# Kernel tuning notes

Hardware: AMD Instinct MI355X
Metric: run time of the kernel (lower is better)

The kernel has to match this reference:

```python
import jax, jax.numpy as jnp
import numpy as np

N, M, E = 100000, 500, 300000
XS, GS, OUT, HEADS = 100, 100, 100, 2
SLOPE = 0.2
EPS = 1e-12


def l2norm(x, axis):
    n = jnp.linalg.norm(x, axis=axis, keepdims=True)
    return x / jnp.maximum(n, EPS)


def gat_layer(h_ijk, ends, n, W, att):
    # W: [heads*out, in_dim] (no bias); att: [1, heads, out]
    heads, out = att.shape[1], att.shape[2]
    c = (h_ijk @ W.T).reshape(-1, heads, out)               # [E, H, D]
    a = jnp.sum(att * c, axis=2, keepdims=True)             # [E, H, 1]
    e = jnp.exp(-jax.nn.leaky_relu(a, SLOPE))
    denom = jax.ops.segment_sum(e, ends, num_segments=n)    # [n, H, 1]
    alpha = e / denom[ends]                                 # segment softmax (dropout=eval/identity)
    h = jax.ops.segment_sum(alpha * c, ends, num_segments=n)  # [n, H, D]
    h = jax.nn.elu(h)
    h = l2norm(h, axis=2)
    return h.reshape(n, heads * out)


def merge_layer(h_in, h_out, Wi, bi, Wo, bo, Wl, bl):
    hi = h_in @ Wi.T + bi
    ho = h_out @ Wo.T + bo
    lam = jax.nn.sigmoid(jnp.concatenate([hi, ho], axis=1) @ Wl.T + bl)
    h = lam * hi + (1.0 - lam) * ho
    return l2norm(jax.nn.elu(h), axis=1)


def setup_inputs() -> dict:
    key = jax.random.key(0)
    ks = jax.random.split(key, 24)
    D = HEADS * OUT  # 200
    in1 = 2 * XS + GS   # 300
    in2 = 3 * D         # 600
    s = 0.05
    return {
        'edge_idx': jax.random.randint(ks[0], (2, E), 0, N),
        'edge_type': jax.random.randint(ks[1], (E,), 0, M),
        'path_idx': jax.random.randint(ks[2], (2, 8), 0, N),
        'path_type': jax.random.randint(ks[3], (2, 8), 0, M),
        'use_path': 0,
        'x': jax.random.normal(ks[4], (N, XS), jnp.float32),
        'g': jax.random.normal(ks[5], (M, GS), jnp.float32),
        'W_in1': s * jax.random.normal(ks[6], (D, in1), jnp.float32),
        'att_in1': s * jax.random.normal(ks[7], (1, HEADS, OUT), jnp.float32),
        'W_out1': s * jax.random.normal(ks[8], (D, in1), jnp.float32),
        'att_out1': s * jax.random.normal(ks[9], (1, HEADS, OUT), jnp.float32),
        'Wi1': s * jax.random.normal(ks[10], (D, D), jnp.float32), 'bi1': jnp.zeros((D,), jnp.float32),
        'Wo1': s * jax.random.normal(ks[11], (D, D), jnp.float32), 'bo1': jnp.zeros((D,), jnp.float32),
        'Wl1': s * jax.random.normal(ks[12], (1, 2 * D), jnp.float32), 'bl1': jnp.zeros((1,), jnp.float32),
        'Wr': s * jax.random.normal(ks[13], (D, GS), jnp.float32), 'br': jnp.zeros((D,), jnp.float32),
        'Wf': s * jax.random.normal(ks[14], (D, in1), jnp.float32), 'bf': jnp.zeros((D,), jnp.float32),
        'W_in2': s * jax.random.normal(ks[15], (D, in2), jnp.float32),
        'att_in2': s * jax.random.normal(ks[16], (1, 1, D), jnp.float32),
        'W_out2': s * jax.random.normal(ks[17], (D, in2), jnp.float32),
        'att_out2': s * jax.random.normal(ks[18], (1, 1, D), jnp.float32),
        'Wi2': s * jax.random.normal(ks[19], (D, D), jnp.float32), 'bi2': jnp.zeros((D,), jnp.float32),
        'Wo2': s * jax.random.normal(ks[20], (D, D), jnp.float32), 'bo2': jnp.zeros((D,), jnp.float32),
        'Wl2': s * jax.random.normal(ks[21], (1, 2 * D), jnp.float32), 'bl2': jnp.zeros((1,), jnp.float32),
        'W_ent': s * jax.random.normal(ks[22], (D, XS), jnp.float32),
    }


def reference(edge_idx, edge_type, path_idx, path_type, use_path, x, g,
              W_in1, att_in1, W_out1, att_out1, Wi1, bi1, Wo1, bo1, Wl1, bl1,
              Wr, br, Wf, bf,
              W_in2, att_in2, W_out2, att_out2, Wi2, bi2, Wo2, bo2, Wl2, bl2,
              W_ent):
    n, m = x.shape[0], g.shape[0]
    x = l2norm(x, axis=1)  # x_initial is renormalized each forward
    row, col = edge_idx[0], edge_idx[1]
    # hop 1: gather-concat per-edge features [E, 2*XS+GS]
    h_ijk = jnp.concatenate([x[row], x[col], g[edge_type]], axis=1)
    h_in = gat_layer(h_ijk, col, n, W_in1, att_in1)
    h_out = gat_layer(h_ijk, row, n, W_out1, att_out1)
    h = merge_layer(h_in, h_out, Wi1, bi1, Wo1, bo1, Wl1, bl1)
    # relation layer
    g_edges = jax.ops.segment_sum(h_ijk, edge_type, num_segments=m)
    g_edges = jax.nn.elu(l2norm(g_edges, axis=1))
    g_prime = (g @ Wr.T + br) + (g_edges @ Wf.T + bf)
    # hop 2
    h_ijk2 = jnp.concatenate([h[row], h[col], g_prime[edge_type]], axis=1)
    h_in2 = gat_layer(h_ijk2, col, n, W_in2, att_in2)
    h_out2 = gat_layer(h_ijk2, row, n, W_out2, att_out2)
    h = merge_layer(h_in2, h_out2, Wi2, bi2, Wo2, bo2, Wl2, bl2)
    # entity residual layer
    h_prime = x @ W_ent.T + h
    return h_prime
```

## Files before the change

### kernel.cpp

```cpp
#include <hip/hip_runtime.h>
#include <cstddef>
#include <cstdint>

#define WSLOPE 0.2f
#define WEPS 1e-12f

typedef __attribute__((ext_vector_type(8))) short bf16x8;
typedef __attribute__((ext_vector_type(4))) float f32x4;

__device__ __forceinline__ float waveSum(float v) {
#pragma unroll
    for (int off = 32; off > 0; off >>= 1) v += __shfl_xor(v, off, 64);
    return v;
}
__device__ __forceinline__ float rowSum16(float v) {
#pragma unroll
    for (int off = 8; off > 0; off >>= 1) v += __shfl_xor(v, off, 64);
    return v;
}
__device__ __forceinline__ float eluf(float v) { return v > 0.f ? v : expm1f(v); }
__device__ __forceinline__ short f2bf(float f) {
    union { float f; uint32_t u; } v; v.f = f;
    uint32_t r = v.u + 0x7FFF + ((v.u >> 16) & 1);
    return (short)(r >> 16);
}
__device__ __forceinline__ float bf2f(short s) {
    union { uint32_t u; float f; } v; v.u = ((uint32_t)(uint16_t)s) << 16;
    return v.f;
}

__global__ void k_nodeprep(const float* __restrict__ x, float* __restrict__ invn,
                           short* __restrict__ xnb,
                           const float* __restrict__ wai, const float* __restrict__ wao,
                           float* __restrict__ rdi, float* __restrict__ cdi,
                           float* __restrict__ rdo, float* __restrict__ cdo, int N) {
    int wid = blockIdx.x * 4 + (threadIdx.x >> 6);
    int lane = threadIdx.x & 63;
    if (wid >= N) return;
    const float* p = x + (size_t)wid * 100;
    float a0 = p[lane];
    float a1 = (lane < 36) ? p[lane + 64] : 0.f;
    float ss = waveSum(a0 * a0 + a1 * a1);
    float inv = 1.f / fmaxf(sqrtf(ss), WEPS);
    if (lane == 0) invn[wid] = inv;
    float f0 = a0 * inv, f1 = a1 * inv;
    short* xb = xnb + (size_t)wid * 112;
    xb[lane] = f2bf(f0);
    if (lane < 36) xb[64 + lane] = f2bf(f1);
    else if (lane < 48) xb[64 + lane] = 0;
#pragma unroll
    for (int h = 0; h < 2; ++h) {
        const float* wi = wai + h * 300;
        const float* wo = wao + h * 300;
        float ri = f0 * wi[lane] + f1 * wi[lane + 64];
        float ci = f0 * wi[100 + lane] + f1 * wi[100 + lane + 64];
        float ro = f0 * wo[lane] + f1 * wo[lane + 64];
        float co = f0 * wo[100 + lane] + f1 * wo[100 + lane + 64];
        ri = waveSum(ri); ci = waveSum(ci); ro = waveSum(ro); co = waveSum(co);
        if (lane == 0) { rdi[wid * 2 + h] = ri; cdi[wid * 2 + h] = ci; rdo[wid * 2 + h] = ro; cdo[wid * 2 + h] = co; }
    }
}

__global__ void k_gprep(const float* __restrict__ g, short* __restrict__ gbf,
                        short* __restrict__ gcomb,
                        const float* __restrict__ wai, const float* __restrict__ wao,
                        float* __restrict__ gdi, float* __restrict__ gdo, int M) {
    int m = blockIdx.x * 4 + (threadIdx.x >> 6);
    int lane = threadIdx.x & 63;
    if (m >= M) return;
    const float* gm = g + (size_t)m * 100;
    float v0 = gm[lane];
    float v1 = (lane < 36) ? gm[lane + 64] : 0.f;
    short b0 = f2bf(v0), b1 = (lane < 36) ? f2bf(v1) : (short)0;
    short* gb = gbf + (size_t)m * 112;
    gb[lane] = b0;
    if (lane < 48) gb[64 + lane] = (lane < 36) ? b1 : (short)0;
    short* gc = gcomb + (size_t)m * 448;
    gc[lane] = b0;
    gc[64 + lane] = b1;
    float s0 = v0 * wai[200 + lane];
    float s1 = v0 * wai[500 + lane];
    float s2 = v0 * wao[200 + lane];
    float s3 = v0 * wao[500 + lane];
    if (lane < 36) {
        s0 += v1 * wai[264 + lane]; s1 += v1 * wai[564 + lane];
        s2 += v1 * wao[264 + lane]; s3 += v1 * wao[564 + lane];
    }
    s0 = waveSum(s0); s1 = waveSum(s1); s2 = waveSum(s2); s3 = waveSum(s3);
    if (lane == 0) { gdi[m * 2] = s0; gdi[m * 2 + 1] = s1; gdo[m * 2] = s2; gdo[m * 2 + 1] = s3; }
}

__global__ void k_count(const int* __restrict__ keys, int* __restrict__ cnt, int n) {
    int i = blockIdx.x * 256 + threadIdx.x;
    if (i < n) atomicAdd(&cnt[keys[i]], 1);
}

#define SCAN_CHUNK 2048
__global__ void k_blocksum(const int* __restrict__ cnt, int* __restrict__ bsum, int n) {
    __shared__ int sh[256];
    int b = blockIdx.x, t = threadIdx.x;
    int base = b * SCAN_CHUNK;
    int s = 0;
    for (int i = t; i < SCAN_CHUNK; i += 256) { int idx = base + i; if (idx < n) s += cnt[idx]; }
    sh[t] = s; __syncthreads();
    for (int off = 128; off > 0; off >>= 1) { if (t < off) sh[t] += sh[t + off]; __syncthreads(); }
    if (t == 0) bsum[b] = sh[0];
}

__global__ void k_scanwrite(const int* __restrict__ cnt, const int* __restrict__ bsum,
                            int* __restrict__ offs, int* __restrict__ cur, int n, int nb) {
    __shared__ int sh[256];
    __shared__ int sbase;
    int b = blockIdx.x, t = threadIdx.x;
    if (t == 0) { int s = 0; for (int i = 0; i < b; ++i) s += bsum[i]; sbase = s; }
    __syncthreads();
    int base = b * SCAN_CHUNK;
    int loc[8]; int ts = 0;
#pragma unroll
    for (int i = 0; i < 8; ++i) { int idx = base + t * 8 + i; int v = (idx < n) ? cnt[idx] : 0; loc[i] = ts; ts += v; }
    sh[t] = ts; __syncthreads();
    for (int off = 1; off < 256; off <<= 1) {
        int v = (t >= off) ? sh[t - off] : 0;
        __syncthreads();
        sh[t] += v;
        __syncthreads();
    }
    int excl = (t == 0) ? 0 : sh[t - 1];
    int gbase = sbase + excl;
#pragma unroll
    for (int i = 0; i < 8; ++i) {
        int idx = base + t * 8 + i;
        if (idx < n) { offs[idx] = gbase + loc[i]; cur[idx] = gbase + loc[i]; }
    }
    if (b == nb - 1 && t == 255) offs[n] = sbase + sh[255];
}

__global__ void k_scatter3(const int* __restrict__ keys, const int* __restrict__ other,
                           const int* __restrict__ et, int* __restrict__ cur,
                           int* __restrict__ nbrS, int* __restrict__ etS,
                           int* __restrict__ keyS, int n) {
    int i = blockIdx.x * 256 + threadIdx.x;
    if (i < n) {
        int p = atomicAdd(&cur[keys[i]], 1);
        nbrS[p] = other[i];
        etS[p] = et[i];
        keyS[p] = keys[i];
    }
}

__global__ void k_scatter2(const int* __restrict__ keys, int* __restrict__ cur,
                           int* __restrict__ rs, int* __restrict__ cs,
                           const int* __restrict__ row, const int* __restrict__ col, int n) {
    int i = blockIdx.x * 256 + threadIdx.x;
    if (i < n) {
        int p = atomicAdd(&cur[keys[i]], 1);
        rs[p] = row[i];
        cs[p] = col[i];
    }
}

__global__ void k_watt(const float* __restrict__ att, const float* __restrict__ W,
                       float* __restrict__ wa, int H, int DH, int K) {
    int id = blockIdx.x * 256 + threadIdx.x;
    if (id >= H * K) return;
    int h = id / K, k = id % K;
    float s = 0.f;
    for (int j = 0; j < DH; ++j) s += att[h * DH + j] * W[(size_t)(h * DH + j) * K + k];
    wa[id] = s;
}

__global__ void k_ew2(const int* __restrict__ nbi, const int* __restrict__ kyi,
                      const int* __restrict__ eti,
                      const int* __restrict__ nbo, const int* __restrict__ kyo,
                      const int* __restrict__ eto,
                      const float* __restrict__ rdi, const float* __restrict__ cdi,
                      const float* __restrict__ rdo, const float* __restrict__ cdo,
                      const float* __restrict__ gdi, const float* __restrict__ gdo,
                      float* __restrict__ ewi, float* __restrict__ ewo, int E, int H) {
    int id = blockIdx.x * 256 + threadIdx.x;
    int tot = E * H;
    if (id >= 2 * tot) return;
    if (id < tot) {
        int p = id / H, h = id - p * H;
        float a = rdi[nbi[p] * H + h] + cdi[kyi[p] * H + h] + gdi[eti[p] * H + h];
        float lr = a > 0.f ? a : WSLOPE * a;
        ewi[id] = expf(-lr);
    } else {
        int id2 = id - tot;
        int p = id2 / H, h = id2 - p * H;
        float a = cdo[nbo[p] * H + h] + rdo[kyo[p] * H + h] + gdo[eto[p] * H + h];
        float lr = a > 0.f ? a : WSLOPE * a;
        ewo[id2] = expf(-lr);
    }
}

template<bool HOP2>
__global__ void k_agg(const int* __restrict__ offs, const int* __restrict__ nbrS,
                      const int* __restrict__ etS, const float* __restrict__ ewS,
                      const short* __restrict__ featB, const short* __restrict__ gB,
                      short* __restrict__ A, int n0, int n1) {
    constexpr int H = HOP2 ? 1 : 2;
    constexpr int LDA = HOP2 ? 672 : 576;
    constexpr int FW = HOP2 ? 224 : 112;
    constexpr int GW = HOP2 ? 224 : 112;
    int node = n0 + blockIdx.x * 4 + (threadIdx.x >> 6);
    int lane = threadIdx.x & 63;
    if (node >= n1) return;
    int o = offs[node];
    int deg = offs[node + 1] - o;
    float va[7];
#pragma unroll
    for (int m = 0; m < 7; ++m) va[m] = 0.f;
    if (deg > 0) {
        float s0 = 0.f, s1 = 0.f;
        for (int i = lane; i < deg; i += 64) {
            s0 += ewS[(size_t)(o + i) * H];
            if (H == 2) s1 += ewS[(size_t)(o + i) * H + 1];
        }
        s0 = waveSum(s0);
        float rd0 = 1.f / s0, rd1 = rd0;
        if (H == 2) { s1 = waveSum(s1); rd1 = 1.f / s1; }
        for (int j = 0; j < deg; ++j) {
            float a0 = ewS[(size_t)(o + j) * H] * rd0;
            float a1 = (H == 2) ? ewS[(size_t)(o + j) * H + 1] * rd1 : a0;
            int nbr = nbrS[o + j];
            int et = etS[o + j];
            const short* fr = featB + (size_t)nbr * FW;
            const short* gr = gB + (size_t)et * GW;
            if (!HOP2) {
#pragma unroll
                for (int m = 0; m < 7; ++m) {
                    int d = lane + m * 64;
                    if (d < 100) va[m] += a0 * bf2f(fr[d]);
                    else if (d < 200) va[m] += a1 * bf2f(fr[d - 100]);
                    else if (d < 300) va[m] += a0 * bf2f(gr[d - 200]);
                    else if (d < 400) va[m] += a1 * bf2f(gr[d - 300]);
                }
            } else {
#pragma unroll
                for (int m = 0; m < 7; ++m) {
                    int d = lane + m * 64;
                    if (d < 200) va[m] += a0 * bf2f(fr[d]);
                    else if (d < 424) va[m] += a0 * bf2f(gr[d - 200]);
                }
            }
        }
    }
    size_t rb = (size_t)(node - n0);
    short* Ar = A + rb * LDA;
    if (!HOP2) {
#pragma unroll
        for (int m = 0; m < 7; ++m) {
            int d = lane + m * 64;
            if (d < 400) {
                int col = d < 100 ? d : (d < 200 ? d + 12 : (d < 300 ? d + 24 : d + 36));
                Ar[col] = f2bf(va[m]);
            }
        }
        if (lane < 48) { int q = lane / 12; int rm = lane - q * 12; Ar[q * 112 + 100 + rm] = 0; }
        const short* sf = featB + (size_t)node * 112;
#pragma unroll
        for (int mm = 0; mm < 2; ++mm) {
            int k = lane + mm * 64;
            if (k < 128) Ar[448 + k] = (deg > 0 && k < 112) ? sf[k] : (short)0;
        }
    } else {
#pragma unroll
        for (int m = 0; m < 7; ++m) {
            int d = lane + m * 64;
            if (d < 424) Ar[d < 200 ? d : d + 24] = f2bf(va[m]);
        }
        if (lane < 24) Ar[200 + lane] = 0;
        const short* sf = featB + (size_t)node * 224;
#pragma unroll
        for (int mm = 0; mm < 4; ++mm) {
            int k = lane + mm * 64;
            if (k < 224) Ar[448 + k] = deg > 0 ? sf[k] : (short)0;
        }
    }
}

template<int KSTEPS, int H, bool HOP1>
__launch_bounds__(256)
__global__ void k_gatmerge(const short* __restrict__ Ain, const short* __restrict__ Aout,
                           const short* __restrict__ WcA, const short* __restrict__ WcB,
                           const short* __restrict__ Wi, const short* __restrict__ Wo,
                           const float* __restrict__ bi, const float* __restrict__ bo,
                           const float* __restrict__ Wl, const float* __restrict__ bl,
                           const short* __restrict__ xnb, const short* __restrict__ Went,
                           float* __restrict__ outf, short* __restrict__ h1b,
                           const float* __restrict__ wa2i, const float* __restrict__ wa2o,
                           float* __restrict__ rdi, float* __restrict__ cdi,
                           float* __restrict__ rdo, float* __restrict__ cdo,
                           int rows) {
    constexpr int LDA = KSTEPS * 32;
    __shared__ short pL[2][64][232];
    const int t = threadIdx.x;
    const int wv = t >> 6, l = t & 63;
    const int lhi = l >> 4, llo = l & 15;
    const int rbase = blockIdx.x * 64 + wv * 16;

#pragma unroll 1
    for (int dir = 0; dir < 2; ++dir) {
        const short* A = dir ? Aout : Ain;
        const short* Wc = dir ? WcB : WcA;
        f32x4 acc[13];
#pragma unroll
        for (int j = 0; j < 13; ++j) acc[j] = f32x4{0.f, 0.f, 0.f, 0.f};
        const short* arow = A + (size_t)(rbase + llo) * LDA + lhi * 8;
#pragma unroll
        for (int kt = 0; kt < KSTEPS; ++kt) {
            bf16x8 a = *(const bf16x8*)(arow + kt * 32);
#pragma unroll
            for (int j = 0; j < 13; ++j) {
                bf16x8 b = *(const bf16x8*)(Wc + (size_t)(j * 16 + llo) * LDA + kt * 32 + lhi * 8);
                acc[j] = __builtin_amdgcn_mfma_f32_16x16x32_bf16(a, b, acc[j], 0, 0, 0);
            }
        }
#pragma unroll
        for (int e = 0; e < 4; ++e) {
            float v[13];
            float s0 = 0.f, s1 = 0.f;
#pragma unroll
            for (int j = 0; j < 13; ++j) {
                int d = j * 16 + llo;
                if (d < 200) {
                    float xv = eluf(acc[j][e]);
                    v[j] = xv;
                    if (H == 1 || d < 100) s0 += xv * xv; else s1 += xv * xv;
                }
            }
            s0 = rowSum16(s0);
            float inv0 = 1.f / fmaxf(sqrtf(s0), WEPS);
            float inv1 = inv0;
            if (H == 2) { s1 = rowSum16(s1); inv1 = 1.f / fmaxf(sqrtf(s1), WEPS); }
            short* pr = &pL[dir][wv * 16 + lhi * 4 + e][0];
#pragma unroll
            for (int j = 0; j < 13; ++j) {
                int d = j * 16 + llo;
                if (d < 200) pr[d] = f2bf(v[j] * ((H == 2 && d >= 100) ? inv1 : inv0));
                else pr[d] = 0;
            }
            pr[208 + llo] = 0;
        }
    }
    __syncthreads();

    f32x4 accA[13], accB[13];
#pragma unroll
    for (int j = 0; j < 13; ++j) { accA[j] = f32x4{0.f, 0.f, 0.f, 0.f}; accB[j] = f32x4{0.f, 0.f, 0.f, 0.f}; }
    const short* pa = &pL[0][wv * 16 + llo][0];
    const short* pb = &pL[1][wv * 16 + llo][0];
#pragma unroll
    for (int kt = 0; kt < 7; ++kt) {
        bf16x8 a1 = *(const bf16x8*)(pa + kt * 32 + lhi * 8);
        bf16x8 a2 = *(const bf16x8*)(pb + kt * 32 + lhi * 8);
#pragma unroll
        for (int j = 0; j < 13; ++j) {
            bf16x8 b1 = *(const bf16x8*)(Wi + (size_t)(j * 16 + llo) * 224 + kt * 32 + lhi * 8);
            accA[j] = __builtin_amdgcn_mfma_f32_16x16x32_bf16(a1, b1, accA[j], 0, 0, 0);
            bf16x8 b2 = *(const bf16x8*)(Wo + (size_t)(j * 16 + llo) * 224 + kt * 32 + lhi * 8);
            accB[j] = __builtin_amdgcn_mfma_f32_16x16x32_bf16(a2, b2, accB[j], 0, 0, 0);
        }
    }
    f32x4 accR[13];
    if (!HOP1) {
#pragma unroll
        for (int j = 0; j < 13; ++j) accR[j] = f32x4{0.f, 0.f, 0.f, 0.f};
        const short* xr = xnb + (size_t)(rbase + llo) * 112 + lhi * 8;
#pragma unroll
        for (int kt = 0; kt < 4; ++kt) {
            bf16x8 a = *(const bf16x8*)(xr + kt * 32);
#pragma unroll
            for (int j = 0; j < 13; ++j) {
                bf16x8 b = *(const bf16x8*)(Went + (size_t)(j * 16 + llo) * 128 + kt * 32 + lhi * 8);
                accR[j] = __builtin_amdgcn_mfma_f32_16x16x32_bf16(a, b, accR[j], 0, 0, 0);
            }
        }
    }

    const int r0 = rbase + lhi * 4;
    float blv = bl[0];
#pragma unroll
    for (int e = 0; e < 4; ++e) {
        int r = r0 + e;
        if (r >= rows) continue;
        float vi[13], vo[13];
        float lp = 0.f;
#pragma unroll
        for (int j = 0; j < 13; ++j) {
            int d = j * 16 + llo;
            if (d < 200) {
                vi[j] = accA[j][e] + bi[d];
                vo[j] = accB[j][e] + bo[d];
                lp += Wl[d] * vi[j] + Wl[200 + d] * vo[j];
            }
        }
        lp = rowSum16(lp);
        float lam = 1.f / (1.f + expf(-(lp + blv)));
        float hv[13];
        float ss = 0.f;
#pragma unroll
        for (int j = 0; j < 13; ++j) {
            int d = j * 16 + llo;
            if (d < 200) { hv[j] = eluf(lam * vi[j] + (1.f - lam) * vo[j]); ss += hv[j] * hv[j]; }
        }
        ss = rowSum16(ss);
        float inv = 1.f / fmaxf(sqrtf(ss), WEPS);
        float ri = 0.f, ci = 0.f, ro = 0.f, co = 0.f;
#pragma unroll
        for (int j = 0; j < 13; ++j) {
            int d = j * 16 + llo;
            if (d < 200) {
                float val = hv[j] * inv;
                if (HOP1) {
                    h1b[(size_t)r * 224 + d] = f2bf(val);
                    ri += val * wa2i[d]; ci += val * wa2i[200 + d];
                    ro += val * wa2o[d]; co += val * wa2o[200 + d];
                } else {
                    outf[(size_t)r * 200 + d] = val + accR[j][e];
                }
            } else if (HOP1) {
                h1b[(size_t)r * 224 + d] = 0;
            }
        }
        if (HOP1) {
            h1b[(size_t)r * 224 + 208 + llo] = 0;
            ri = rowSum16(ri); ci = rowSum16(ci); ro = rowSum16(ro); co = rowSum16(co);
            if (llo == 0) { rdi[r] = ri; cdi[r] = ci; rdo[r] = ro; cdo[r] = co; }
        }
    }
}

__launch_bounds__(256)
__global__ void k_mgemm_rel(const short* __restrict__ A, const short* __restrict__ Wb,
                            const float* __restrict__ brf,
                            short* __restrict__ gout, const float* __restrict__ wai,
                            const float* __restrict__ wao,
                            float* __restrict__ gdi, float* __restrict__ gdo, int rows) {
    constexpr int KSTEPS = 14, LDW = KSTEPS * 32;
    const int t = threadIdx.x;
    const int wv = t >> 6, l = t & 63;
    const int lhi = l >> 4, llo = l & 15;
    const int rbase = blockIdx.x * 64 + wv * 16;
    f32x4 acc[13];
#pragma unroll
    for (int j = 0; j < 13; ++j) acc[j] = f32x4{0.f, 0.f, 0.f, 0.f};
    const short* arow = A + (size_t)(rbase + llo) * 448 + lhi * 8;
#pragma unroll
    for (int kt = 0; kt < KSTEPS; ++kt) {
        bf16x8 a = *(const bf16x8*)(arow + kt * 32);
#pragma unroll
        for (int j = 0; j < 13; ++j) {
            bf16x8 b = *(const bf16x8*)(Wb + (size_t)(j * 16 + llo) * LDW + kt * 32 + lhi * 8);
            acc[j] = __builtin_amdgcn_mfma_f32_16x16x32_bf16(a, b, acc[j], 0, 0, 0);
        }
    }
    const int r0 = rbase + lhi * 4;
#pragma unroll
    for (int e = 0; e < 4; ++e) {
        int r = r0 + e;
        if (r >= rows) continue;
        short* pr = gout + (size_t)r * 224;
        float gi = 0.f, go = 0.f;
#pragma unroll
        for (int j = 0; j < 13; ++j) {
            int d = j * 16 + llo;
            if (d < 200) {
                float val = acc[j][e] + brf[d];
                pr[d] = f2bf(val);
                gi += val * wai[400 + d];
                go += val * wao[400 + d];
            } else {
                pr[d] = 0;
            }
        }
        pr[208 + llo] = 0;
        gi = rowSum16(gi); go = rowSum16(go);
        if (llo == 0) { gdi[r] = gi; gdo[r] = go; }
    }
}

__global__ void k_prepw(const float* __restrict__ W, int ldW, int koff, int Klen, int span,
                        int mode, short* __restrict__ Wb, int ldWb, int dst) {
    int id = blockIdx.x * 256 + threadIdx.x;
    int tot = 208 * span;
    if (id >= tot) return;
    int d = id / span, k = id - d * span;
    float v = 0.f;
    if (d < 200) {
        if (mode == 0) { if (k < Klen) v = W[(size_t)d * ldW + koff + k]; }
        else { int h = d / 100; int kk = k - h * 112; if (kk >= 0 && kk < Klen) v = W[(size_t)d * ldW + koff + kk]; }
    }
    Wb[(size_t)d * ldWb + dst + k] = f2bf(v);
}

__global__ void k_prepwrf(const float* __restrict__ Wr, const float* __restrict__ Wf,
                          short* __restrict__ Wb) {
    int id = blockIdx.x * 256 + threadIdx.x;
    if (id >= 208 * 448) return;
    int d = id / 448, k = id - d * 448;
    float v = 0.f;
    if (d < 200) {
        if (k < 100) v = Wr[(size_t)d * 100 + k];
        else if (k >= 128 && k < 428) v = Wf[(size_t)d * 300 + (k - 128)];
    }
    Wb[id] = f2bf(v);
}

__global__ void k_brf(const float* __restrict__ br, const float* __restrict__ bf,
                      float* __restrict__ brf) {
    int d = threadIdx.x;
    if (d < 200) brf[d] = br[d] + bf[d];
}

__global__ void k_gedges_b(const int* __restrict__ rsT, const int* __restrict__ csT,
                           const int* __restrict__ offsT,
                           const float* __restrict__ x, const float* __restrict__ invn,
                           const float* __restrict__ g, short* __restrict__ gcomb, int M) {
    __shared__ float red[6];
    int m = blockIdx.x, t = threadIdx.x;
    int o = offsT[m];
    int deg = offsT[m + 1] - o;
    float acc = 0.f;
    if (t < 128) {
        int d = t; bool ok = d < 100;
        for (int i = 0; i < deg; ++i) {
            int r = rsT[o + i];
            if (ok) acc += x[(size_t)r * 100 + d] * invn[r];
        }
    } else if (t < 256) {
        int d = t - 128; bool ok = d < 100;
        for (int i = 0; i < deg; ++i) {
            int c = csT[o + i];
            if (ok) acc += x[(size_t)c * 100 + d] * invn[c];
        }
    } else {
        int d = t - 256;
        if (d < 100) acc = (float)deg * g[(size_t)m * 100 + d];
    }
    float sq = waveSum(acc * acc);
    if ((t & 63) == 0) red[t >> 6] = sq;
    __syncthreads();
    float s2 = red[0] + red[1] + red[2] + red[3] + red[4] + red[5];
    float inv = 1.f / fmaxf(sqrtf(s2), WEPS);
    short* orow = gcomb + (size_t)m * 448 + 128;
    if (t < 128) {
        if (t < 100) orow[t] = f2bf(eluf(acc * inv));
    } else if (t < 256) {
        int d = t - 128;
        if (d < 100) orow[100 + d] = f2bf(eluf(acc * inv));
    } else {
        int d = t - 256;
        if (d < 100) orow[200 + d] = f2bf(eluf(acc * inv));
        else if (d < 120) orow[200 + d] = 0;
    }
}

extern "C" void kernel_launch(void* const* d_in, const int* in_sizes, int n_in,
                              void* d_out, int out_size, void* d_ws, size_t ws_size,
                              hipStream_t stream) {
    const int* eidx   = (const int*)d_in[0];
    const int* etype  = (const int*)d_in[1];
    const float* x    = (const float*)d_in[5];
    const float* g    = (const float*)d_in[6];
    const float* W_in1  = (const float*)d_in[7];
    const float* att_in1 = (const float*)d_in[8];
    const float* W_out1 = (const float*)d_in[9];
    const float* att_out1 = (const float*)d_in[10];
    const float* Wi1 = (const float*)d_in[11]; const float* bi1 = (const float*)d_in[12];
    const float* Wo1 = (const float*)d_in[13]; const float* bo1 = (const float*)d_in[14];
    const float* Wl1 = (const float*)d_in[15]; const float* bl1 = (const float*)d_in[16];
    const float* Wr  = (const float*)d_in[17]; const float* br  = (const float*)d_in[18];
    const float* Wf  = (const float*)d_in[19]; const float* bf  = (const float*)d_in[20];
    const float* W_in2  = (const float*)d_in[21]; const float* att_in2 = (const float*)d_in[22];
    const float* W_out2 = (const float*)d_in[23]; const float* att_out2 = (const float*)d_in[24];
    const float* Wi2 = (const float*)d_in[25]; const float* bi2 = (const float*)d_in[26];
    const float* Wo2 = (const float*)d_in[27]; const float* bo2 = (const float*)d_in[28];
    const float* Wl2 = (const float*)d_in[29]; const float* bl2 = (const float*)d_in[30];
    const float* W_ent = (const float*)d_in[31];

    const int E = in_sizes[1];
    const int N = in_sizes[5] / 100;
    const int M = in_sizes[6] / 100;
    const int Mr = (M + 63) & ~63;
    float* out = (float*)d_out;
    const int* row = eidx;
    const int* col = eidx + E;

    char* w = (char*)d_ws;
    size_t off_b = 0;
    auto alloc = [&](size_t bytes) -> void* {
        void* p = w + off_b;
        off_b += (bytes + 255) & ~(size_t)255;
        return p;
    };
    float* invn  = (float*)alloc((size_t)N * 4);
    short* h1_bf = (short*)alloc((size_t)(N + 64) * 224 * 2);
    short* xn_bf = (short*)alloc((size_t)(N + 64) * 112 * 2);
    short* g_bf  = (short*)alloc((size_t)M * 112 * 2);
    short* gp_bf = (short*)alloc((size_t)Mr * 224 * 2);
    int* offs_in = (int*)alloc((size_t)(N + 1) * 4);
    int* offs_out= (int*)alloc((size_t)(N + 1) * 4);
    int* offsT   = (int*)alloc((size_t)(M + 1) * 4);
    int* nbrS_in = (int*)alloc((size_t)E * 4);
    int* etS_in  = (int*)alloc((size_t)E * 4);
    int* keyS_in = (int*)alloc((size_t)E * 4);
    int* nbrS_out= (int*)alloc((size_t)E * 4);
    int* etS_out = (int*)alloc((size_t)E * 4);
    int* keyS_out= (int*)alloc((size_t)E * 4);
    int* rsT     = (int*)alloc((size_t)E * 4);
    int* csT     = (int*)alloc((size_t)E * 4);
    int* cnt     = (int*)alloc((size_t)N * 4);
    int* cur     = (int*)alloc((size_t)N * 4);
    int* bsum    = (int*)alloc((size_t)64 * 4);
    float* wa1_in = (float*)alloc((size_t)640 * 4);
    float* wa1_out= (float*)alloc((size_t)640 * 4);
    float* wa2_in = (float*)alloc((size_t)640 * 4);
    float* wa2_out= (float*)alloc((size_t)640 * 4);
    float* rdot_in = (float*)alloc((size_t)N * 2 * 4);
    float* cdot_in = (float*)alloc((size_t)N * 2 * 4);
    float* rdot_out= (float*)alloc((size_t)N * 2 * 4);
    float* cdot_out= (float*)alloc((size_t)N * 2 * 4);
    float* gdot_in = (float*)alloc((size_t)M * 2 * 4);
    float* gdot_out= (float*)alloc((size_t)M * 2 * 4);
    float* ewS_in  = (float*)alloc((size_t)E * 2 * 4);
    float* ewS_out = (float*)alloc((size_t)E * 2 * 4);
    short* gcomb   = (short*)alloc((size_t)Mr * 448 * 2);
    short* Wc_in1  = (short*)alloc((size_t)208 * 576 * 2);
    short* Wc_out1 = (short*)alloc((size_t)208 * 576 * 2);
    short* Wc_in2  = (short*)alloc((size_t)208 * 672 * 2);
    short* Wc_out2 = (short*)alloc((size_t)208 * 672 * 2);
    short* Wm_i1   = (short*)alloc((size_t)208 * 224 * 2);
    short* Wm_o1   = (short*)alloc((size_t)208 * 224 * 2);
    short* Wm_i2   = (short*)alloc((size_t)208 * 224 * 2);
    short* Wm_o2   = (short*)alloc((size_t)208 * 224 * 2);
    short* Wb_ent  = (short*)alloc((size_t)208 * 128 * 2);
    short* Wrf_b   = (short*)alloc((size_t)208 * 448 * 2);
    float* brf     = (float*)alloc((size_t)200 * 4);

    if (off_b >= ws_size) return;
    size_t rem = ws_size - off_b;
    long long Cll = (long long)(rem / 2816);
    long long Nr64 = ((long long)N + 63) & ~63LL;
    int C = (int)(Cll > Nr64 ? Nr64 : Cll);
    C &= ~63;
    if (C < 64) return;
    short* Ac0 = (short*)alloc((size_t)C * 672 * 2);
    short* Ac1 = (short*)alloc((size_t)C * 672 * 2);
    if (off_b > ws_size) return;

    const int gE = (E + 255) / 256;
    const int gN4 = (N + 3) / 4;
    const int gM4 = (M + 3) / 4;
    const int gM64 = (M + 63) / 64;

    auto gsp = [](int span) { return (208 * span + 255) / 256; };
    k_prepw<<<gsp(224), 256, 0, stream>>>(W_in1, 300, 0, 100, 224, 1, Wc_in1, 576, 0);
    k_prepw<<<gsp(224), 256, 0, stream>>>(W_in1, 300, 200, 100, 224, 1, Wc_in1, 576, 224);
    k_prepw<<<gsp(128), 256, 0, stream>>>(W_in1, 300, 100, 100, 128, 0, Wc_in1, 576, 448);
    k_prepw<<<gsp(224), 256, 0, stream>>>(W_out1, 300, 100, 100, 224, 1, Wc_out1, 576, 0);
    k_prepw<<<gsp(224), 256, 0, stream>>>(W_out1, 300, 200, 100, 224, 1, Wc_out1, 576, 224);
    k_prepw<<<gsp(128), 256, 0, stream>>>(W_out1, 300, 0, 100, 128, 0, Wc_out1, 576, 448);
    k_prepw<<<gsp(224), 256, 0, stream>>>(W_in2, 600, 0, 200, 224, 0, Wc_in2, 672, 0);
    k_prepw<<<gsp(224), 256, 0, stream>>>(W_in2, 600, 400, 200, 224, 0, Wc_in2, 672, 224);
    k_prepw<<<gsp(224), 256, 0, stream>>>(W_in2, 600, 200, 200, 224, 0, Wc_in2, 672, 448);
    k_prepw<<<gsp(224), 256, 0, stream>>>(W_out2, 600, 200, 200, 224, 0, Wc_out2, 672, 0);
    k_prepw<<<gsp(224), 256, 0, stream>>>(W_out2, 600, 400, 200, 224, 0, Wc_out2, 672, 224);
    k_prepw<<<gsp(224), 256, 0, stream>>>(W_out2, 600, 0, 200, 224, 0, Wc_out2, 672, 448);
    k_prepw<<<gsp(224), 256, 0, stream>>>(Wi1, 200, 0, 200, 224, 0, Wm_i1, 224, 0);
    k_prepw<<<gsp(224), 256, 0, stream>>>(Wo1, 200, 0, 200, 224, 0, Wm_o1, 224, 0);
    k_prepw<<<gsp(224), 256, 0, stream>>>(Wi2, 200, 0, 200, 224, 0, Wm_i2, 224, 0);
    k_prepw<<<gsp(224), 256, 0, stream>>>(Wo2, 200, 0, 200, 224, 0, Wm_o2, 224, 0);
    k_prepw<<<gsp(128), 256, 0, stream>>>(W_ent, 100, 0, 100, 128, 0, Wb_ent, 128, 0);
    k_prepwrf<<<gsp(448), 256, 0, stream>>>(Wr, Wf, Wrf_b);
    k_brf<<<1, 256, 0, stream>>>(br, bf, brf);

    int nbN = (N + SCAN_CHUNK - 1) / SCAN_CHUNK;
    int nbM = (M + SCAN_CHUNK - 1) / SCAN_CHUNK;
    hipMemsetAsync(cnt, 0, (size_t)N * 4, stream);
    k_count<<<gE, 256, 0, stream>>>(col, cnt, E);
    k_blocksum<<<nbN, 256, 0, stream>>>(cnt, bsum, N);
    k_scanwrite<<<nbN, 256, 0, stream>>>(cnt, bsum, offs_in, cur, N, nbN);
    k_scatter3<<<gE, 256, 0, stream>>>(col, row, etype, cur, nbrS_in, etS_in, keyS_in, E);

    hipMemsetAsync(cnt, 0, (size_t)N * 4, stream);
    k_count<<<gE, 256, 0, stream>>>(row, cnt, E);
    k_blocksum<<<nbN, 256, 0, stream>>>(cnt, bsum, N);
    k_scanwrite<<<nbN, 256, 0, stream>>>(cnt, bsum, offs_out, cur, N, nbN);
    k_scatter3<<<gE, 256, 0, stream>>>(row, col, etype, cur, nbrS_out, etS_out, keyS_out, E);

    hipMemsetAsync(cnt, 0, (size_t)M * 4, stream);
    k_count<<<gE, 256, 0, stream>>>(etype, cnt, E);
    k_blocksum<<<nbM, 256, 0, stream>>>(cnt, bsum, M);
    k_scanwrite<<<nbM, 256, 0, stream>>>(cnt, bsum, offsT, cur, M, nbM);
    k_scatter2<<<gE, 256, 0, stream>>>(etype, cur, rsT, csT, row, col, E);

    k_watt<<<(600 + 255) / 256, 256, 0, stream>>>(att_in1, W_in1, wa1_in, 2, 100, 300);
    k_watt<<<(600 + 255) / 256, 256, 0, stream>>>(att_out1, W_out1, wa1_out, 2, 100, 300);
    k_watt<<<(600 + 255) / 256, 256, 0, stream>>>(att_in2, W_in2, wa2_in, 1, 200, 600);
    k_watt<<<(600 + 255) / 256, 256, 0, stream>>>(att_out2, W_out2, wa2_out, 1, 200, 600);

    k_nodeprep<<<gN4, 256, 0, stream>>>(x, invn, xn_bf, wa1_in, wa1_out,
                                        rdot_in, cdot_in, rdot_out, cdot_out, N);
    k_gprep<<<gM4, 256, 0, stream>>>(g, g_bf, gcomb, wa1_in, wa1_out, gdot_in, gdot_out, M);
    k_ew2<<<(2 * E * 2 + 255) / 256, 256, 0, stream>>>(nbrS_in, keyS_in, etS_in,
                                                       nbrS_out, keyS_out, etS_out,
                                                       rdot_in, cdot_in, rdot_out, cdot_out,
                                                       gdot_in, gdot_out, ewS_in, ewS_out, E, 2);

    for (int n0 = 0; n0 < N; n0 += C) {
        int rows = (N - n0 < C) ? (N - n0) : C;
        int n1 = n0 + rows;
        int ga = (rows + 3) / 4;
        int gb = (rows + 63) / 64;
        k_agg<false><<<ga, 256, 0, stream>>>(offs_in, nbrS_in, etS_in, ewS_in, xn_bf, g_bf, Ac0, n0, n1);
        k_agg<false><<<ga, 256, 0, stream>>>(offs_out, nbrS_out, etS_out, ewS_out, xn_bf, g_bf, Ac1, n0, n1);
        k_gatmerge<18, 2, true><<<gb, 256, 0, stream>>>(Ac0, Ac1, Wc_in1, Wc_out1, Wm_i1, Wm_o1,
                                                        bi1, bo1, Wl1, bl1, nullptr, nullptr,
                                                        nullptr, h1_bf + (size_t)n0 * 224,
                                                        wa2_in, wa2_out,
                                                        rdot_in + n0, cdot_in + n0,
                                                        rdot_out + n0, cdot_out + n0, rows);
    }

    k_gedges_b<<<M, 384, 0, stream>>>(rsT, csT, offsT, x, invn, g, gcomb, M);
    k_mgemm_rel<<<gM64, 256, 0, stream>>>(gcomb, Wrf_b, brf, gp_bf, wa2_in, wa2_out, gdot_in, gdot_out, M);

    k_ew2<<<(2 * E + 255) / 256, 256, 0, stream>>>(nbrS_in, keyS_in, etS_in,
                                                   nbrS_out, keyS_out, etS_out,
                                                   rdot_in, cdot_in, rdot_out, cdot_out,
                                                   gdot_in, gdot_out, ewS_in, ewS_out, E, 1);

    for (int n0 = 0; n0 < N; n0 += C) {
        int rows = (N - n0 < C) ? (N - n0) : C;
        int n1 = n0 + rows;
        int ga = (rows + 3) / 4;
        int gb = (rows + 63) / 64;
        k_agg<true><<<ga, 256, 0, stream>>>(offs_in, nbrS_in, etS_in, ewS_in, h1_bf, gp_bf, Ac0, n0, n1);
        k_agg<true><<<ga, 256, 0, stream>>>(offs_out, nbrS_out, etS_out, ewS_out, h1_bf, gp_bf, Ac1, n0, n1);
        k_gatmerge<21, 1, false><<<gb, 256, 0, stream>>>(Ac0, Ac1, Wc_in2, Wc_out2, Wm_i2, Wm_o2,
                                                         bi2, bo2, Wl2, bl2,
                                                         xn_bf + (size_t)n0 * 112, Wb_ent,
                                                         out + (size_t)n0 * 200, nullptr,
                                                         nullptr, nullptr,
                                                         nullptr, nullptr, nullptr, nullptr, rows);
    }
}
```

Before: 3.079 ms.

## Split fused GAT+merge kernel into per-direction GEMM and column-split merge kernel

```diff
diff --git a/kernel.cpp b/kernel.cpp
--- a/kernel.cpp
+++ b/kernel.cpp
@@ -280,10 +280,60 @@
     }
 }
 
-template<int KSTEPS, int H, bool HOP1>
+template<int KSTEPS, int H>
 __launch_bounds__(256)
-__global__ void k_gatmerge(const short* __restrict__ Ain, const short* __restrict__ Aout,
-                           const short* __restrict__ WcA, const short* __restrict__ WcB,
+__global__ void k_mgemm_post(const short* __restrict__ A, const short* __restrict__ Wb,
+                             short* __restrict__ post, int rows, int lda) {
+    constexpr int LDW = KSTEPS * 32;
+    const int t = threadIdx.x;
+    const int wv = t >> 6, l = t & 63;
+    const int lhi = l >> 4, llo = l & 15;
+    const int rbase = blockIdx.x * 64 + wv * 16;
+    f32x4 acc[13];
+#pragma unroll
+    for (int j = 0; j < 13; ++j) acc[j] = f32x4{0.f, 0.f, 0.f, 0.f};
+    const short* arow = A + (size_t)(rbase + llo) * lda + lhi * 8;
+#pragma unroll
+    for (int kt = 0; kt < KSTEPS; ++kt) {
+        bf16x8 a = *(const bf16x8*)(arow + kt * 32);
+#pragma unroll
+        for (int j = 0; j < 13; ++j) {
+            bf16x8 b = *(const bf16x8*)(Wb + (size_t)(j * 16 + llo) * LDW + kt * 32 + lhi * 8);
+            acc[j] = __builtin_amdgcn_mfma_f32_16x16x32_bf16(a, b, acc[j], 0, 0, 0);
+        }
+    }
+    const int r0 = rbase + lhi * 4;
+#pragma unroll
+    for (int e = 0; e < 4; ++e) {
+        int r = r0 + e;
+        if (r >= rows) continue;
+        float v[13];
+        float s0 = 0.f, s1 = 0.f;
+#pragma unroll
+        for (int j = 0; j < 13; ++j) {
+            int d = j * 16 + llo;
+            if (d < 200) {
+                float xv = eluf(acc[j][e]);
+                v[j] = xv;
+                if (H == 1 || d < 100) s0 += xv * xv; else s1 += xv * xv;
+            }
+        }
+        s0 = rowSum16(s0);
+        float inv0 = 1.f / fmaxf(sqrtf(s0), WEPS);
+        float inv1 = inv0;
+        if (H == 2) { s1 = rowSum16(s1); inv1 = 1.f / fmaxf(sqrtf(s1), WEPS); }
+        short* pr = post + (size_t)r * 224;
+#pragma unroll
+        for (int j = 0; j < 13; ++j) {
+            int d = j * 16 + llo;
+            if (d < 200) pr[d] = f2bf(v[j] * ((H == 2 && d >= 100) ? inv1 : inv0));
+        }
+    }
+}
+
+template<bool HOP1>
+__launch_bounds__(512)
+__global__ void k_mergemm2(const short* __restrict__ pA, const short* __restrict__ pB,
                            const short* __restrict__ Wi, const short* __restrict__ Wo,
                            const float* __restrict__ bi, const float* __restrict__ bo,
                            const float* __restrict__ Wl, const float* __restrict__ bl,
@@ -293,126 +343,104 @@
                            float* __restrict__ rdi, float* __restrict__ cdi,
                            float* __restrict__ rdo, float* __restrict__ cdo,
                            int rows) {
-    constexpr int LDA = KSTEPS * 32;
-    __shared__ short pL[2][64][232];
+    __shared__ float lpS[2][64];
+    __shared__ float ssS[2][64];
+    __shared__ float dotS[2][64][4];
     const int t = threadIdx.x;
-    const int wv = t >> 6, l = t & 63;
+    const int wvAll = t >> 6;
+    const int rg = wvAll >> 1;
+    const int half = wvAll & 1;
+    const int l = t & 63;
     const int lhi = l >> 4, llo = l & 15;
-    const int rbase = blockIdx.x * 64 + wv * 16;
-
-#pragma unroll 1
-    for (int dir = 0; dir < 2; ++dir) {
-        const short* A = dir ? Aout : Ain;
-        const short* Wc = dir ? WcB : WcA;
-        f32x4 acc[13];
-#pragma unroll
-        for (int j = 0; j < 13; ++j) acc[j] = f32x4{0.f, 0.f, 0.f, 0.f};
-        const short* arow = A + (size_t)(rbase + llo) * LDA + lhi * 8;
-#pragma unroll
-        for (int kt = 0; kt < KSTEPS; ++kt) {
-            bf16x8 a = *(const bf16x8*)(arow + kt * 32);
-#pragma unroll
-            for (int j = 0; j < 13; ++j) {
-                bf16x8 b = *(const bf16x8*)(Wc + (size_t)(j * 16 + llo) * LDA + kt * 32 + lhi * 8);
-                acc[j] = __builtin_amdgcn_mfma_f32_16x16x32_bf16(a, b, acc[j], 0, 0, 0);
-            }
-        }
-#pragma unroll
-        for (int e = 0; e < 4; ++e) {
-            float v[13];
-            float s0 = 0.f, s1 = 0.f;
-#pragma unroll
-            for (int j = 0; j < 13; ++j) {
-                int d = j * 16 + llo;
-                if (d < 200) {
-                    float xv = eluf(acc[j][e]);
-                    v[j] = xv;
-                    if (H == 1 || d < 100) s0 += xv * xv; else s1 += xv * xv;
-                }
-            }
-            s0 = rowSum16(s0);
-            float inv0 = 1.f / fmaxf(sqrtf(s0), WEPS);
-            float inv1 = inv0;
-            if (H == 2) { s1 = rowSum16(s1); inv1 = 1.f / fmaxf(sqrtf(s1), WEPS); }
-            short* pr = &pL[dir][wv * 16 + lhi * 4 + e][0];
-#pragma unroll
-            for (int j = 0; j < 13; ++j) {
-                int d = j * 16 + llo;
-                if (d < 200) pr[d] = f2bf(v[j] * ((H == 2 && d >= 100) ? inv1 : inv0));
-                else pr[d] = 0;
-            }
-            pr[208 + llo] = 0;
-        }
-    }
-    __syncthreads();
-
-    f32x4 accA[13], accB[13];
-#pragma unroll
-    for (int j = 0; j < 13; ++j) { accA[j] = f32x4{0.f, 0.f, 0.f, 0.f}; accB[j] = f32x4{0.f, 0.f, 0.f, 0.f}; }
-    const short* pa = &pL[0][wv * 16 + llo][0];
-    const short* pb = &pL[1][wv * 16 + llo][0];
+    const int jbase = half * 7;
+    const int rbase = blockIdx.x * 64 + rg * 16;
+    f32x4 accA[7], accB[7];
+#pragma unroll
+    for (int j = 0; j < 7; ++j) { accA[j] = f32x4{0.f, 0.f, 0.f, 0.f}; accB[j] = f32x4{0.f, 0.f, 0.f, 0.f}; }
+    const short* pa = pA + (size_t)(rbase + llo) * 224 + lhi * 8;
+    const short* pb = pB + (size_t)(rbase + llo) * 224 + lhi * 8;
 #pragma unroll
     for (int kt = 0; kt < 7; ++kt) {
-        bf16x8 a1 = *(const bf16x8*)(pa + kt * 32 + lhi * 8);
-        bf16x8 a2 = *(const bf16x8*)(pb + kt * 32 + lhi * 8);
-#pragma unroll
-        for (int j = 0; j < 13; ++j) {
-            bf16x8 b1 = *(const bf16x8*)(Wi + (size_t)(j * 16 + llo) * 224 + kt * 32 + lhi * 8);
-            accA[j] = __builtin_amdgcn_mfma_f32_16x16x32_bf16(a1, b1, accA[j], 0, 0, 0);
-            bf16x8 b2 = *(const bf16x8*)(Wo + (size_t)(j * 16 + llo) * 224 + kt * 32 + lhi * 8);
-            accB[j] = __builtin_amdgcn_mfma_f32_16x16x32_bf16(a2, b2, accB[j], 0, 0, 0);
-        }
-    }
-    f32x4 accR[13];
+        bf16x8 a1 = *(const bf16x8*)(pa + kt * 32);
+        bf16x8 a2 = *(const bf16x8*)(pb + kt * 32);
+#pragma unroll
+        for (int j = 0; j < 7; ++j) {
+            if (jbase + j < 13) {
+                bf16x8 b1 = *(const bf16x8*)(Wi + (size_t)((jbase + j) * 16 + llo) * 224 + kt * 32 + lhi * 8);
+                accA[j] = __builtin_amdgcn_mfma_f32_16x16x32_bf16(a1, b1, accA[j], 0, 0, 0);
+                bf16x8 b2 = *(const bf16x8*)(Wo + (size_t)((jbase + j) * 16 + llo) * 224 + kt * 32 + lhi * 8);
+                accB[j] = __builtin_amdgcn_mfma_f32_16x16x32_bf16(a2, b2, accB[j], 0, 0, 0);
+            }
+        }
+    }
+    f32x4 accR[7];
     if (!HOP1) {
 #pragma unroll
-        for (int j = 0; j < 13; ++j) accR[j] = f32x4{0.f, 0.f, 0.f, 0.f};
+        for (int j = 0; j < 7; ++j) accR[j] = f32x4{0.f, 0.f, 0.f, 0.f};
         const short* xr = xnb + (size_t)(rbase + llo) * 112 + lhi * 8;
 #pragma unroll
         for (int kt = 0; kt < 4; ++kt) {
             bf16x8 a = *(const bf16x8*)(xr + kt * 32);
 #pragma unroll
-            for (int j = 0; j < 13; ++j) {
-                bf16x8 b = *(const bf16x8*)(Went + (size_t)(j * 16 + llo) * 128 + kt * 32 + lhi * 8);
-                accR[j] = __builtin_amdgcn_mfma_f32_16x16x32_bf16(a, b, accR[j], 0, 0, 0);
-            }
-        }
-    }
-
+            for (int j = 0; j < 7; ++j) {
+                if (jbase + j < 13) {
+                    bf16x8 b = *(const bf16x8*)(Went + (size_t)((jbase + j) * 16 + llo) * 128 + kt * 32 + lhi * 8);
+                    accR[j] = __builtin_amdgcn_mfma_f32_16x16x32_bf16(a, b, accR[j], 0, 0, 0);
+                }
+            }
+        }
+    }
     const int r0 = rbase + lhi * 4;
+    const int rrb = rg * 16 + lhi * 4;
     float blv = bl[0];
+#pragma unroll
+    for (int e = 0; e < 4; ++e) {
+        float lp = 0.f;
+#pragma unroll
+        for (int j = 0; j < 7; ++j) {
+            int d = (jbase + j) * 16 + llo;
+            if (jbase + j < 13 && d < 200)
+                lp += Wl[d] * (accA[j][e] + bi[d]) + Wl[200 + d] * (accB[j][e] + bo[d]);
+        }
+        lp = rowSum16(lp);
+        if (llo == 0) lpS[half][rrb + e] = lp;
+    }
+    __syncthreads();
+    float lamAll[4];
+#pragma unroll
+    for (int e = 0; e < 4; ++e) {
+        float lam = 1.f / (1.f + expf(-(lpS[0][rrb + e] + lpS[1][rrb + e] + blv)));
+        lamAll[e] = lam;
+        float ss = 0.f;
+#pragma unroll
+        for (int j = 0; j < 7; ++j) {
+            int d = (jbase + j) * 16 + llo;
+            if (jbase + j < 13 && d < 200) {
+                float vi = accA[j][e] + bi[d];
+                float vo = accB[j][e] + bo[d];
+                float hv = eluf(lam * vi + (1.f - lam) * vo);
+                ss += hv * hv;
+            }
+        }
+        ss = rowSum16(ss);
+        if (llo == 0) ssS[half][rrb + e] = ss;
+    }
+    __syncthreads();
 #pragma unroll
     for (int e = 0; e < 4; ++e) {
         int r = r0 + e;
         if (r >= rows) continue;
-        float vi[13], vo[13];
-        float lp = 0.f;
-#pragma unroll
-        for (int j = 0; j < 13; ++j) {
-            int d = j * 16 + llo;
+        float inv = 1.f / fmaxf(sqrtf(ssS[0][rrb + e] + ssS[1][rrb + e]), WEPS);
+        float lam = lamAll[e];
+        float ri = 0.f, ci = 0.f, ro = 0.f, co = 0.f;
+#pragma unroll
+        for (int j = 0; j < 7; ++j) {
+            if (jbase + j >= 13) continue;
+            int d = (jbase + j) * 16 + llo;
             if (d < 200) {
-                vi[j] = accA[j][e] + bi[d];
-                vo[j] = accB[j][e] + bo[d];
-                lp += Wl[d] * vi[j] + Wl[200 + d] * vo[j];
-            }
-        }
-        lp = rowSum16(lp);
-        float lam = 1.f / (1.f + expf(-(lp + blv)));
-        float hv[13];
-        float ss = 0.f;
-#pragma unroll
-        for (int j = 0; j < 13; ++j) {
-            int d = j * 16 + llo;
-            if (d < 200) { hv[j] = eluf(lam * vi[j] + (1.f - lam) * vo[j]); ss += hv[j] * hv[j]; }
-        }
-        ss = rowSum16(ss);
-        float inv = 1.f / fmaxf(sqrtf(ss), WEPS);
-        float ri = 0.f, ci = 0.f, ro = 0.f, co = 0.f;
-#pragma unroll
-        for (int j = 0; j < 13; ++j) {
-            int d = j * 16 + llo;
-            if (d < 200) {
-                float val = hv[j] * inv;
+                float vi = accA[j][e] + bi[d];
+                float vo = accB[j][e] + bo[d];
+                float val = eluf(lam * vi + (1.f - lam) * vo) * inv;
                 if (HOP1) {
                     h1b[(size_t)r * 224 + d] = f2bf(val);
                     ri += val * wa2i[d]; ci += val * wa2i[200 + d];
@@ -425,9 +453,27 @@
             }
         }
         if (HOP1) {
-            h1b[(size_t)r * 224 + 208 + llo] = 0;
+            if (half) h1b[(size_t)r * 224 + 208 + llo] = 0;
             ri = rowSum16(ri); ci = rowSum16(ci); ro = rowSum16(ro); co = rowSum16(co);
-            if (llo == 0) { rdi[r] = ri; cdi[r] = ci; rdo[r] = ro; cdo[r] = co; }
+            if (llo == 0) {
+                dotS[half][rrb + e][0] = ri; dotS[half][rrb + e][1] = ci;
+                dotS[half][rrb + e][2] = ro; dotS[half][rrb + e][3] = co;
+            }
+        }
+    }
+    if (HOP1) {
+        __syncthreads();
+        if (half == 0 && llo == 0) {
+#pragma unroll
+            for (int e = 0; e < 4; ++e) {
+                int r = r0 + e;
+                if (r < rows) {
+                    rdi[r] = dotS[0][rrb + e][0] + dotS[1][rrb + e][0];
+                    cdi[r] = dotS[0][rrb + e][1] + dotS[1][rrb + e][1];
+                    rdo[r] = dotS[0][rrb + e][2] + dotS[1][rrb + e][2];
+                    cdo[r] = dotS[0][rrb + e][3] + dotS[1][rrb + e][3];
+                }
+            }
         }
     }
 }
@@ -641,19 +687,24 @@
 
     if (off_b >= ws_size) return;
     size_t rem = ws_size - off_b;
-    long long Cll = (long long)(rem / 2816);
+    long long Cll = (long long)(rem / 3712);
     long long Nr64 = ((long long)N + 63) & ~63LL;
     int C = (int)(Cll > Nr64 ? Nr64 : Cll);
     C &= ~63;
     if (C < 64) return;
-    short* Ac0 = (short*)alloc((size_t)C * 672 * 2);
-    short* Ac1 = (short*)alloc((size_t)C * 672 * 2);
+    short* Ac0   = (short*)alloc((size_t)C * 672 * 2);
+    short* Ac1   = (short*)alloc((size_t)C * 672 * 2);
+    short* postA = (short*)alloc((size_t)C * 224 * 2);
+    short* postB = (short*)alloc((size_t)C * 224 * 2);
     if (off_b > ws_size) return;
 
     const int gE = (E + 255) / 256;
     const int gN4 = (N + 3) / 4;
     const int gM4 = (M + 3) / 4;
     const int gM64 = (M + 63) / 64;
+
+    hipMemsetAsync(postA, 0, (size_t)C * 224 * 2, stream);
+    hipMemsetAsync(postB, 0, (size_t)C * 224 * 2, stream);
 
     auto gsp = [](int span) { return (208 * span + 255) / 256; };
     k_prepw<<<gsp(224), 256, 0, stream>>>(W_in1, 300, 0, 100, 224, 1, Wc_in1, 576, 0);
@@ -716,12 +767,14 @@
         int gb = (rows + 63) / 64;
         k_agg<false><<<ga, 256, 0, stream>>>(offs_in, nbrS_in, etS_in, ewS_in, xn_bf, g_bf, Ac0, n0, n1);
         k_agg<false><<<ga, 256, 0, stream>>>(offs_out, nbrS_out, etS_out, ewS_out, xn_bf, g_bf, Ac1, n0, n1);
-        k_gatmerge<18, 2, true><<<gb, 256, 0, stream>>>(Ac0, Ac1, Wc_in1, Wc_out1, Wm_i1, Wm_o1,
-                                                        bi1, bo1, Wl1, bl1, nullptr, nullptr,
-                                                        nullptr, h1_bf + (size_t)n0 * 224,
-                                                        wa2_in, wa2_out,
-                                                        rdot_in + n0, cdot_in + n0,
-                                                        rdot_out + n0, cdot_out + n0, rows);
+        k_mgemm_post<18, 2><<<gb, 256, 0, stream>>>(Ac0, Wc_in1, postA, rows, 576);
+        k_mgemm_post<18, 2><<<gb, 256, 0, stream>>>(Ac1, Wc_out1, postB, rows, 576);
+        k_mergemm2<true><<<gb, 512, 0, stream>>>(postA, postB, Wm_i1, Wm_o1, bi1, bo1, Wl1, bl1,
+                                                 nullptr, nullptr,
+                                                 nullptr, h1_bf + (size_t)n0 * 224,
+                                                 wa2_in, wa2_out,
+                                                 rdot_in + n0, cdot_in + n0,
+                                                 rdot_out + n0, cdot_out + n0, rows);
     }
 
     k_gedges_b<<<M, 384, 0, stream>>>(rsT, csT, offsT, x, invn, g, gcomb, M);
@@ -739,11 +792,12 @@
         int gb = (rows + 63) / 64;
         k_agg<true><<<ga, 256, 0, stream>>>(offs_in, nbrS_in, etS_in, ewS_in, h1_bf, gp_bf, Ac0, n0, n1);
         k_agg<true><<<ga, 256, 0, stream>>>(offs_out, nbrS_out, etS_out, ewS_out, h1_bf, gp_bf, Ac1, n0, n1);
-        k_gatmerge<21, 1, false><<<gb, 256, 0, stream>>>(Ac0, Ac1, Wc_in2, Wc_out2, Wm_i2, Wm_o2,
-                                                         bi2, bo2, Wl2, bl2,
-                                                         xn_bf + (size_t)n0 * 112, Wb_ent,
-                                                         out + (size_t)n0 * 200, nullptr,
-                                                         nullptr, nullptr,
-                                                         nullptr, nullptr, nullptr, nullptr, rows);
-    }
-}
+        k_mgemm_post<21, 1><<<gb, 256, 0, stream>>>(Ac0, Wc_in2, postA, rows, 672);
+        k_mgemm_post<21, 1><<<gb, 256, 0, stream>>>(Ac1, Wc_out2, postB, rows, 672);
+        k_mergemm2<false><<<gb, 512, 0, stream>>>(postA, postB, Wm_i2, Wm_o2, bi2, bo2, Wl2, bl2,
+                                                  xn_bf + (size_t)n0 * 112, Wb_ent,
+                                                  out + (size_t)n0 * 200, nullptr,
+                                                  nullptr, nullptr,
+                                                  nullptr, nullptr, nullptr, nullptr, rows);
+    }
+}
```

After: 2.535 ms. 1.21x faster.
